# Kernel optimization log

Hardware: AMD Instinct MI355X
Metric: run time of the kernel (lower is better)

## Reference

```python
import jax, jax.numpy as jnp
import numpy as np

K_BITS = 128  # hash bits (k in __init__)
WORD = 32     # pack bits into uint32 words -> K_BITS // WORD = 4 words


def _pack_bits(bits_u32):
    # bits_u32: [N, K_BITS] uint32 in {0,1} -> [N, K_BITS//WORD] uint32 keys
    N = bits_u32.shape[0]
    b = bits_u32.reshape(N, K_BITS // WORD, WORD)
    shifts = jnp.arange(WORD, dtype=jnp.uint32)
    return jnp.sum(jnp.left_shift(b, shifts), axis=-1, dtype=jnp.uint32)  # [N, 4]


def setup_inputs() -> dict:
    key = jax.random.key(0)
    k1, k2 = jax.random.split(key)
    T, B, D = 128, 64, 4096
    latent_state = jax.random.normal(k1, (T, B, D), dtype=jnp.float32)
    A = jax.random.normal(k2, (K_BITS, D), dtype=jnp.float32)  # fixed random projection buffer
    return {"latent_state": latent_state, "A": A}


def reference(latent_state, A):
    # latent_state: [T, B, D]; A: [k, D]. Returns intrinsic reward [T, B].
    T, B, D = latent_state.shape
    flat = latent_state.reshape(T * B, D)                    # detach is a no-op for fwd
    proj = flat @ A.T                                        # [N, k]
    bits = (proj > 0).astype(jnp.uint32)                     # SimHash sign bits
    words = _pack_bits(bits)                                 # [N, 4] collision-free 128-bit key

    # counts dict starts empty each run: visit count of row i is the number of
    # rows j <= i with an identical key (keys processed in row order).
    N = words.shape[0]
    eq = jnp.ones((N, N), dtype=bool)
    for w in range(K_BITS // WORD):  # small fixed loop over 4 key words
        eq = eq & (words[:, None, w] == words[None, :, w])
    counts = jnp.tril(eq).sum(axis=1)                        # [N] int, >= 1
    intrinsic = 1.0 / jnp.sqrt(counts.astype(latent_state.dtype))
    return intrinsic.reshape(T, B)
```

## Files before the change

### kernel.cpp

```cpp
#include <hip/hip_runtime.h>
#include <stdint.h>

#define D_DIM 4096
#define N_ROWS 8192

typedef __attribute__((ext_vector_type(8))) short bfrag8;
typedef __attribute__((ext_vector_type(4))) float facc4;
typedef unsigned long long u64;

__device__ __forceinline__ uint32_t pack_bf16x2(float lo, float hi) {
    union { float f; uint32_t u; } a, b;
    a.f = lo; b.f = hi;
    return (b.u & 0xFFFF0000u) | (a.u >> 16);
}

__global__ void __launch_bounds__(256)
prep_A(const float* __restrict__ A, uint32_t* __restrict__ A_sw) {
    const int S = blockIdx.x * 256 + threadIdx.x;
    const int c = S >> 10;
    const int s = S & 1023;
    const int n = s >> 3;
    const int g = (s & 7) ^ (n & 7);
    const float* src = A + (size_t)n * D_DIM + c * 64 + g * 8;
    float4 f0 = *(const float4*)(src);
    float4 f1 = *(const float4*)(src + 4);
    uint4 o;
    o.x = pack_bf16x2(f0.x, f0.y);
    o.y = pack_bf16x2(f0.z, f0.w);
    o.z = pack_bf16x2(f1.x, f1.y);
    o.w = pack_bf16x2(f1.z, f1.w);
    *(uint4*)(A_sw + (size_t)S * 4) = o;
}

__global__ void __launch_bounds__(1024, 4)
gemm_pack_fused(const float* __restrict__ L, const uint32_t* __restrict__ A_sw,
                u64* __restrict__ folded) {
    __shared__ ushort Ls[4][32 * 72];
    __shared__ uint4  As[4][1024];
    __shared__ u64 halves[2][32];

    const int tid  = threadIdx.x;
    const int g    = tid >> 8;
    const int t    = tid & 255;
    const int wg   = t >> 6;
    const int lane = tid & 63;
    const int row0 = blockIdx.x * 32;
    const int c  = lane & 15;
    const int q  = lane >> 4;
    const int wm = wg >> 1;
    const int wn = wg & 1;

    const int lrow = t >> 3;
    const int lf4  = t & 7;
    const float* lsrc = L + (size_t)(row0 + lrow) * D_DIM + g * 1024 + lf4 * 4;
    ushort* ldst = &Ls[g][lrow * 72 + lf4 * 4];

    facc4 acc[4];
#pragma unroll
    for (int i = 0; i < 4; i++) acc[i] = (facc4){0.f, 0.f, 0.f, 0.f};

    for (int kc = 0; kc < 1024; kc += 64) {
        const uint32_t* gA = A_sw + (size_t)((g * 1024 + kc) >> 6) * 4096;
#pragma unroll
        for (int i = 0; i < 4; i++) {
            const int slot0 = wg * 256 + i * 64;
            __builtin_amdgcn_global_load_lds(
                (const __attribute__((address_space(1))) uint32_t*)(gA + (slot0 + lane) * 4),
                (__attribute__((address_space(3))) uint32_t*)(&As[g][slot0]),
                16, 0, 0);
        }
        float4 f0 = *(const float4*)(lsrc + kc);
        float4 f1 = *(const float4*)(lsrc + kc + 32);
        *(uint2*)ldst        = make_uint2(pack_bf16x2(f0.x, f0.y), pack_bf16x2(f0.z, f0.w));
        *(uint2*)(ldst + 32) = make_uint2(pack_bf16x2(f1.x, f1.y), pack_bf16x2(f1.z, f1.w));
        __syncthreads();

#pragma unroll
        for (int ks = 0; ks < 2; ks++) {
            bfrag8 a = *(const bfrag8*)&Ls[g][(16 * wm + c) * 72 + ks * 32 + q * 8];
#pragma unroll
            for (int ct = 0; ct < 4; ct++) {
                const int n  = 64 * wn + 16 * ct + c;
                const int gl = ks * 4 + q;
                bfrag8 b = *(const bfrag8*)&As[g][n * 8 + (gl ^ (n & 7))];
                acc[ct] = __builtin_amdgcn_mfma_f32_16x16x32_bf16(a, b, acc[ct], 0, 0, 0);
            }
        }
        __syncthreads();
    }

    facc4* red = (facc4*)&As[0][0];
    const int sw = (t >> 1) & 7;
    if (g > 0) {
        facc4* dst = red + (g - 1) * 1024;
#pragma unroll
        for (int ct = 0; ct < 4; ct++)
            dst[(t * 4 + ct) ^ sw] = acc[ct];
    }
    __syncthreads();
    if (g == 0) {
#pragma unroll
        for (int s = 0; s < 3; s++) {
            const facc4* src = red + s * 1024;
#pragma unroll
            for (int ct = 0; ct < 4; ct++)
                acc[ct] += src[(t * 4 + ct) ^ sw];
        }
        u64 masks[4][4];
#pragma unroll
        for (int ct = 0; ct < 4; ct++)
#pragma unroll
            for (int r = 0; r < 4; r++)
                masks[ct][r] = __ballot(acc[ct][r] > 0.0f);

        if (lane < 16) {
            const int qq = lane >> 2, r = lane & 3;
            u64 half = 0;
#pragma unroll
            for (int ct = 0; ct < 4; ct++) {
                u64 bits = (masks[ct][r] >> (16 * qq)) & 0xFFFFull;
                half |= bits << (16 * ct);
            }
            halves[wn][16 * wm + lane] = half;
        }
    }
    __syncthreads();
    if (tid < 32)
        folded[row0 + tid] = halves[0][tid] ^ halves[1][tid];
}

__global__ void __launch_bounds__(512)
count_rows(const u64* __restrict__ folded, float* __restrict__ out) {
    __shared__ u64 K[N_ROWS];
    const int tid = threadIdx.x;
    for (int i = tid; i < N_ROWS; i += 512) K[i] = folded[i];
    __syncthreads();

    const int g    = blockIdx.x * 8 + (tid >> 6);
    const int lane = tid & 63;
    int rows[4];
    u64 my[4];
    int cnt[4] = {0, 0, 0, 0};
#pragma unroll
    for (int r = 0; r < 4; r++) {
        rows[r] = g + 2048 * r;
        my[r] = K[rows[r]];
    }
    const int maxrow = rows[3];
    for (int j = lane; j <= maxrow; j += 64) {
        u64 k = K[j];
#pragma unroll
        for (int r = 0; r < 4; r++)
            cnt[r] += (int)((j <= rows[r]) & (k == my[r]));
    }
#pragma unroll
    for (int r = 0; r < 4; r++) {
        int v = cnt[r];
#pragma unroll
        for (int o = 32; o; o >>= 1) v += __shfl_xor(v, o, 64);
        if (lane == 0) out[rows[r]] = rsqrtf((float)v);
    }
}

extern "C" void kernel_launch(void* const* d_in, const int* in_sizes, int n_in,
                              void* d_out, int out_size, void* d_ws, size_t ws_size,
                              hipStream_t stream) {
    const float* latent = (const float*)d_in[0];
    const float* A      = (const float*)d_in[1];
    float* out          = (float*)d_out;

    uint32_t* A_sw = (uint32_t*)d_ws;
    u64* folded = (u64*)((char*)d_ws + (1 << 20));

    prep_A<<<256, 256, 0, stream>>>(A, A_sw);
    gemm_pack_fused<<<256, 1024, 0, stream>>>(latent, A_sw, folded);
    count_rows<<<256, 512, 0, stream>>>(folded, out);
}
```

Baseline: 228.7 us.

## Restructure GEMM to 16-row blocks with per-wave column tiles over full K

Replaces the split-K GEMM (four groups each covering a quarter of D, then an LDS reduction) with smaller 16-row blocks where each of eight waves owns 16 hash columns across the entire D. This removes the cross-group reduction and doubles the grid size to improve occupancy. In exchange every block streams all of A, giving twice the A traffic through L2. Each k-step also does only two MFMAs per wave between barriers, raising sync overhead per unit of compute.

```diff
diff --git a/kernel.cpp b/kernel.cpp
--- a/kernel.cpp
+++ b/kernel.cpp
@@ -32,101 +32,74 @@
     *(uint4*)(A_sw + (size_t)S * 4) = o;
 }
 
-__global__ void __launch_bounds__(1024, 4)
-gemm_pack_fused(const float* __restrict__ L, const uint32_t* __restrict__ A_sw,
-                u64* __restrict__ folded) {
-    __shared__ ushort Ls[4][32 * 72];
-    __shared__ uint4  As[4][1024];
-    __shared__ u64 halves[2][32];
+__global__ void __launch_bounds__(512)
+gemm_pack_n4(const float* __restrict__ L, const uint32_t* __restrict__ A_sw,
+             u64* __restrict__ folded) {
+    __shared__ ushort Ls[16 * 72];
+    __shared__ uint4  As[1024];
+    __shared__ ushort sl[8][16];
 
     const int tid  = threadIdx.x;
-    const int g    = tid >> 8;
-    const int t    = tid & 255;
-    const int wg   = t >> 6;
+    const int wave = tid >> 6;
     const int lane = tid & 63;
-    const int row0 = blockIdx.x * 32;
-    const int c  = lane & 15;
-    const int q  = lane >> 4;
-    const int wm = wg >> 1;
-    const int wn = wg & 1;
+    const int row0 = blockIdx.x * 16;
+    const int c = lane & 15;
+    const int q = lane >> 4;
+    const int g  = wave >> 1;
+    const int wn = wave & 1;
+    const int ncol = 32 * g + 16 * wn + c;
 
-    const int lrow = t >> 3;
-    const int lf4  = t & 7;
-    const float* lsrc = L + (size_t)(row0 + lrow) * D_DIM + g * 1024 + lf4 * 4;
-    ushort* ldst = &Ls[g][lrow * 72 + lf4 * 4];
+    const int srow = (tid >> 4) & 15;
+    const int sf4  = tid & 15;
+    const float* lsrc = L + (size_t)(row0 + srow) * D_DIM + sf4 * 4;
+    ushort* ldst = &Ls[srow * 72 + sf4 * 4];
+    const bool do_ls = (tid < 256);
 
-    facc4 acc[4];
+    facc4 acc = (facc4){0.f, 0.f, 0.f, 0.f};
+
+    for (int kc = 0; kc < D_DIM; kc += 64) {
+        const uint32_t* gA = A_sw + (size_t)(kc >> 6) * 4096;
 #pragma unroll
-    for (int i = 0; i < 4; i++) acc[i] = (facc4){0.f, 0.f, 0.f, 0.f};
-
-    for (int kc = 0; kc < 1024; kc += 64) {
-        const uint32_t* gA = A_sw + (size_t)((g * 1024 + kc) >> 6) * 4096;
-#pragma unroll
-        for (int i = 0; i < 4; i++) {
-            const int slot0 = wg * 256 + i * 64;
+        for (int i = 0; i < 2; i++) {
+            const int slot0 = wave * 128 + i * 64;
             __builtin_amdgcn_global_load_lds(
                 (const __attribute__((address_space(1))) uint32_t*)(gA + (slot0 + lane) * 4),
-                (__attribute__((address_space(3))) uint32_t*)(&As[g][slot0]),
+                (__attribute__((address_space(3))) uint32_t*)(&As[slot0]),
                 16, 0, 0);
         }
-        float4 f0 = *(const float4*)(lsrc + kc);
-        float4 f1 = *(const float4*)(lsrc + kc + 32);
-        *(uint2*)ldst        = make_uint2(pack_bf16x2(f0.x, f0.y), pack_bf16x2(f0.z, f0.w));
-        *(uint2*)(ldst + 32) = make_uint2(pack_bf16x2(f1.x, f1.y), pack_bf16x2(f1.z, f1.w));
+        if (do_ls) {
+            float4 f = *(const float4*)(lsrc + kc);
+            *(uint2*)ldst = make_uint2(pack_bf16x2(f.x, f.y), pack_bf16x2(f.z, f.w));
+        }
         __syncthreads();
 
 #pragma unroll
         for (int ks = 0; ks < 2; ks++) {
-            bfrag8 a = *(const bfrag8*)&Ls[g][(16 * wm + c) * 72 + ks * 32 + q * 8];
-#pragma unroll
-            for (int ct = 0; ct < 4; ct++) {
-                const int n  = 64 * wn + 16 * ct + c;
-                const int gl = ks * 4 + q;
-                bfrag8 b = *(const bfrag8*)&As[g][n * 8 + (gl ^ (n & 7))];
-                acc[ct] = __builtin_amdgcn_mfma_f32_16x16x32_bf16(a, b, acc[ct], 0, 0, 0);
-            }
+            bfrag8 a = *(const bfrag8*)&Ls[c * 72 + ks * 32 + q * 8];
+            const int gl = ks * 4 + q;
+            bfrag8 b = *(const bfrag8*)&As[ncol * 8 + (gl ^ (ncol & 7))];
+            acc = __builtin_amdgcn_mfma_f32_16x16x32_bf16(a, b, acc, 0, 0, 0);
         }
         __syncthreads();
     }
 
-    facc4* red = (facc4*)&As[0][0];
-    const int sw = (t >> 1) & 7;
-    if (g > 0) {
-        facc4* dst = red + (g - 1) * 1024;
+    u64 masks[4];
 #pragma unroll
-        for (int ct = 0; ct < 4; ct++)
-            dst[(t * 4 + ct) ^ sw] = acc[ct];
+    for (int r = 0; r < 4; r++)
+        masks[r] = __ballot(acc[r] > 0.0f);
+
+    if (lane < 16) {
+        const int qq = lane >> 2, r = lane & 3;
+        sl[wave][lane] = (ushort)((masks[r] >> (16 * qq)) & 0xFFFFull);
     }
     __syncthreads();
-    if (g == 0) {
-#pragma unroll
-        for (int s = 0; s < 3; s++) {
-            const facc4* src = red + s * 1024;
-#pragma unroll
-            for (int ct = 0; ct < 4; ct++)
-                acc[ct] += src[(t * 4 + ct) ^ sw];
-        }
-        u64 masks[4][4];
-#pragma unroll
-        for (int ct = 0; ct < 4; ct++)
-#pragma unroll
-            for (int r = 0; r < 4; r++)
-                masks[ct][r] = __ballot(acc[ct][r] > 0.0f);
-
-        if (lane < 16) {
-            const int qq = lane >> 2, r = lane & 3;
-            u64 half = 0;
-#pragma unroll
-            for (int ct = 0; ct < 4; ct++) {
-                u64 bits = (masks[ct][r] >> (16 * qq)) & 0xFFFFull;
-                half |= bits << (16 * ct);
-            }
-            halves[wn][16 * wm + lane] = half;
-        }
+    if (tid < 16) {
+        u64 lo = (u64)sl[0][tid] | ((u64)sl[1][tid] << 16) |
+                 ((u64)sl[2][tid] << 32) | ((u64)sl[3][tid] << 48);
+        u64 hi = (u64)sl[4][tid] | ((u64)sl[5][tid] << 16) |
+                 ((u64)sl[6][tid] << 32) | ((u64)sl[7][tid] << 48);
+        folded[row0 + tid] = lo ^ hi;
     }
-    __syncthreads();
-    if (tid < 32)
-        folded[row0 + tid] = halves[0][tid] ^ halves[1][tid];
 }
 
 __global__ void __launch_bounds__(512)
@@ -173,6 +146,6 @@
     u64* folded = (u64*)((char*)d_ws + (1 << 20));
 
     prep_A<<<256, 256, 0, stream>>>(A, A_sw);
-    gemm_pack_fused<<<256, 1024, 0, stream>>>(latent, A_sw, folded);
+    gemm_pack_n4<<<512, 512, 0, stream>>>(latent, A_sw, folded);
     count_rows<<<256, 512, 0, stream>>>(folded, out);
 }
```

Result: slower. 236.1 us (+3.2%).
